# Performance work log

Measured on AMD Instinct MI355X. Metric: run time of the kernel, lower is better.

## Reference

```python
import jax, jax.numpy as jnp
import numpy as np

S = 64.0
M = 0.5
COS_M = float(np.cos(M))
SIN_M = float(np.sin(M))
MM = float(np.sin(M) * M)
THRESHOLD = float(np.cos(np.pi - M))
B, D, V = 2048, 512, 100000


def setup_inputs() -> dict:
    key = jax.random.key(0)
    k1, k2, k3 = jax.random.split(key, 3)
    embeddings = jax.random.normal(k1, (B, D), dtype=jnp.float32)
    labels = jax.random.randint(k2, (B,), 0, V, dtype=jnp.int64)
    # xavier_uniform for [V, D]: limit = sqrt(6/(fan_in+fan_out))
    limit = float(np.sqrt(6.0 / (D + V)))
    weight = jax.random.uniform(k3, (V, D), minval=-limit, maxval=limit, dtype=jnp.float32)
    return {"embeddings": embeddings, "labels": labels, "weight": weight}


def _l2norm(x, axis):
    # matches F.normalize(p=2, eps=1e-12)
    n = jnp.linalg.norm(x, axis=axis, keepdims=True)
    return x / jnp.maximum(n, 1e-12)


def reference(embeddings, labels, weight):
    e = _l2norm(embeddings, axis=1)          # [B, D]
    w = _l2norm(weight, axis=1)              # [V, D]
    cos_theta = jnp.clip(e @ w.T, -1.0, 1.0)  # [B, V]
    sin_theta = jnp.sqrt(jnp.clip(1.0 - cos_theta * cos_theta, 0.0, 1.0))
    cos_theta_m = cos_theta * COS_M - sin_theta * SIN_M
    cos_theta_m = jnp.where(cos_theta > THRESHOLD, cos_theta_m, cos_theta - MM)
    logits = cos_theta_m * S
    logp = jax.nn.log_softmax(logits, axis=1)
    nll = -jnp.take_along_axis(logp, labels[:, None], axis=1)[:, 0]
    return jnp.mean(nll)
```

## Files before the change

kernel.cpp:

```cpp
#include <hip/hip_runtime.h>
#include <hip/hip_bf16.h>
#include <math.h>

#define B_ 2048
#define D_ 512
#define V_ 100000
#define BM 128
#define BN 128
#define NCT 782
#define NBLK (16 * NCT)
#define NBUF 3
#define RED_STRIDE 20

constexpr float S_SCALE = 64.0f;
constexpr float COS_M_ = 0.8775825618903728f;
constexpr float SIN_M_ = 0.479425538604203f;
constexpr float MM_    = 0.2397127693021015f;
constexpr float THRESH = -0.8775825618903728f;
constexpr float LOG2E  = 1.4426950408889634f;
constexpr float LN2    = 0.6931471805599453f;
constexpr float S2     = 64.0f * LOG2E;
constexpr float CMS2   = COS_M_ * S2;
constexpr float SINM_S2= SIN_M_ * S2;
constexpr float KS2    = SINM_S2 * SINM_S2;
constexpr float MMS2   = MM_ * S2;

typedef __attribute__((ext_vector_type(8))) short short8;
typedef __attribute__((ext_vector_type(4))) float f32x4;
typedef __attribute__((ext_vector_type(2))) long long2_t;

__device__ __forceinline__ unsigned short f2bf(float x) {
    __hip_bfloat16 h = __float2bfloat16(x);
    unsigned short u;
    __builtin_memcpy(&u, &h, 2);
    return u;
}

__device__ __forceinline__ void load_lds16(const void* g, void* l) {
    __builtin_amdgcn_global_load_lds(
        (const __attribute__((address_space(1))) unsigned int*)g,
        (__attribute__((address_space(3))) unsigned int*)l,
        16, 0, 0);
}

__device__ __forceinline__ unsigned int pk_fp8x4(float x, float y, float z, float w) {
    int p = __builtin_amdgcn_cvt_pk_fp8_f32(x, y, 0, false);
    p = __builtin_amdgcn_cvt_pk_fp8_f32(z, w, p, true);
    return (unsigned int)p;
}

__device__ __forceinline__ int permj(int j) {
    return (j & ~15) | (((j >> 1) & 3) << 2) | (((j >> 3) & 1) << 1) | (j & 1);
}

__global__ void k_norm_e(const float* __restrict__ e, unsigned short* __restrict__ ebf,
                         unsigned char* __restrict__ ebf8, float* __restrict__ rne,
                         unsigned int* __restrict__ zbuf) {
    if (zbuf && blockIdx.x == 0) zbuf[threadIdx.x] = 0u;
    int row = blockIdx.x * 4 + (threadIdx.x >> 6);
    int lane = threadIdx.x & 63;
    const float4* src = (const float4*)(e + (size_t)row * D_);
    float4 a = src[lane];
    float4 b = src[lane + 64];
    float ss = a.x*a.x + a.y*a.y + a.z*a.z + a.w*a.w
             + b.x*b.x + b.y*b.y + b.z*b.z + b.w*b.w;
    #pragma unroll
    for (int d = 1; d < 64; d <<= 1) ss += __shfl_xor(ss, d, 64);
    float rn = 1.0f / fmaxf(sqrtf(ss), 1e-12f);
    ushort4* dst = (ushort4*)(ebf + (size_t)row * D_);
    dst[lane]      = make_ushort4(f2bf(a.x*rn), f2bf(a.y*rn), f2bf(a.z*rn), f2bf(a.w*rn));
    dst[lane + 64] = make_ushort4(f2bf(b.x*rn), f2bf(b.y*rn), f2bf(b.z*rn), f2bf(b.w*rn));
    if (ebf8) {
        unsigned int* d8 = (unsigned int*)(ebf8 + (size_t)row * D_);
        d8[permj(lane)]      = pk_fp8x4(a.x*rn, a.y*rn, a.z*rn, a.w*rn);
        d8[permj(lane + 64)] = pk_fp8x4(b.x*rn, b.y*rn, b.z*rn, b.w*rn);
    }
    if (lane == 0) rne[row] = rn;
}

__global__ void k_norm_w(const float* __restrict__ w, float* __restrict__ rnw,
                         unsigned char* __restrict__ wbf8) {
    int row = blockIdx.x * 4 + (threadIdx.x >> 6);
    int lane = threadIdx.x & 63;
    const float4* src = (const float4*)(w + (size_t)row * D_);
    float4 a = src[lane];
    float4 b = src[lane + 64];
    float ss = a.x*a.x + a.y*a.y + a.z*a.z + a.w*a.w
             + b.x*b.x + b.y*b.y + b.z*b.z + b.w*b.w;
    #pragma unroll
    for (int d = 1; d < 64; d <<= 1) ss += __shfl_xor(ss, d, 64);
    float rn = 1.0f / fmaxf(sqrtf(ss), 1e-12f);
    if (wbf8) {
        unsigned int* d8 = (unsigned int*)(wbf8 + (size_t)row * D_);
        d8[permj(lane)]      = pk_fp8x4(a.x*rn, a.y*rn, a.z*rn, a.w*rn);
        d8[permj(lane + 64)] = pk_fp8x4(b.x*rn, b.y*rn, b.z*rn, b.w*rn);
    }
    if (lane == 0) rnw[row] = rn;
}

__global__ __launch_bounds__(256, 3) void k_gemm8(const unsigned char* __restrict__ ebf8,
                                                  const unsigned char* __restrict__ wbf8,
                                                  const unsigned char* __restrict__ zbuf,
                                                  float* __restrict__ partials) {
    const int id = blockIdx.x;
    const int wi = (id & 7) * (NBLK / 8) + (id >> 3);
    const int ct = wi >> 4, rt = wi & 15;
    const int row0 = rt * BM, n0 = ct * BN;
    const int tid = threadIdx.x, lane = tid & 63, wid = tid >> 6;
    const int wm = wid >> 1, wn = wid & 1;

    __shared__ __align__(16) unsigned char lds8[NBUF][16384];
    float* red = (float*)&lds8[0][0];

    f32x4 acc[4][4];
    #pragma unroll
    for (int i = 0; i < 4; ++i)
        #pragma unroll
        for (int j = 0; j < 4; ++j)
            acc[i][j] = (f32x4){0.f, 0.f, 0.f, 0.f};

    const int c_ = (lane & 3) ^ ((lane >> 3) & 3);
    const int r0s = wid * 16 + (lane >> 2);
    const unsigned char* gA0 = ebf8 + (size_t)(row0 + r0s) * D_ + c_ * 16;
    const unsigned char* gA1 = ebf8 + (size_t)(row0 + 64 + r0s) * D_ + c_ * 16;
    int gb0 = n0 + r0s, gb1 = n0 + 64 + r0s;
    const unsigned char* gB0 = (gb0 < V_) ? wbf8 + (size_t)gb0 * D_ + c_ * 16 : zbuf + c_ * 16;
    const unsigned char* gB1 = (gb1 < V_) ? wbf8 + (size_t)gb1 * D_ + c_ * 16 : zbuf + c_ * 16;
    const int lb = wid * 1024;

    auto STAGE = [&](int t) {
        unsigned char* Lb = &lds8[t % NBUF][0];
        const int off = t * 64;
        load_lds16(gA0 + off, Lb + lb);
        load_lds16(gA1 + off, Lb + 4096 + lb);
        load_lds16(gB0 + off, Lb + 8192 + lb);
        load_lds16(gB1 + off, Lb + 12288 + lb);
    };

    const int slot = ((lane >> 4) ^ (((lane & 15) >> 1) & 3)) & 3;
    int aoff[4], boff[4];
    #pragma unroll
    for (int mf = 0; mf < 4; ++mf)
        aoff[mf] = (wm * 64 + mf * 16 + (lane & 15)) * 64 + slot * 16;
    #pragma unroll
    for (int nf = 0; nf < 4; ++nf)
        boff[nf] = 8192 + (wn * 64 + nf * 16 + (lane & 15)) * 64 + slot * 16;

    STAGE(0);
    STAGE(1);
    for (int t = 0; t < 8; ++t) {
        if (t < 7) asm volatile("s_waitcnt vmcnt(4)\n\ts_barrier" ::: "memory");
        else       asm volatile("s_waitcnt vmcnt(0)\n\ts_barrier" ::: "memory");
        if (t + 2 < 8) STAGE(t + 2);

        const char* Lb = (const char*)&lds8[t % NBUF][0];
        long2_t a2[4], b2[4];
        #pragma unroll
        for (int mf = 0; mf < 4; ++mf) a2[mf] = *(const long2_t*)(Lb + aoff[mf]);
        #pragma unroll
        for (int nf = 0; nf < 4; ++nf) b2[nf] = *(const long2_t*)(Lb + boff[nf]);
        #pragma unroll
        for (int mf = 0; mf < 4; ++mf)
            #pragma unroll
            for (int nf = 0; nf < 4; ++nf) {
                acc[mf][nf] = __builtin_amdgcn_mfma_f32_16x16x32_fp8_fp8(a2[mf].x, b2[nf].x, acc[mf][nf], 0, 0, 0);
                acc[mf][nf] = __builtin_amdgcn_mfma_f32_16x16x32_fp8_fp8(a2[mf].y, b2[nf].y, acc[mf][nf], 0, 0, 0);
            }
    }
    __syncthreads();

    #pragma unroll
    for (int mf = 0; mf < 4; ++mf) {
        #pragma unroll
        for (int r = 0; r < 4; ++r) {
            float vsum = 0.0f;
            #pragma unroll
            for (int nf = 0; nf < 4; ++nf) {
                float c = acc[mf][nf][r];
                c = __builtin_amdgcn_fmed3f(c, -1.0f, 1.0f);
                float tt = fmaf(-c, c, 1.0f);
                float sts = __builtin_amdgcn_sqrtf(tt * KS2);
                float lgm = fmaf(c, CMS2, -sts);
                float lga = fmaf(c, S2, -MMS2);
                float lg = (c > THRESH) ? lgm : lga;
                vsum += __builtin_amdgcn_exp2f(lg);
            }
            int rowloc = wm * 64 + mf * 16 + (lane >> 4) * 4 + r;
            red[(wn * BM + rowloc) * RED_STRIDE + (lane & 15)] = vsum;
        }
    }
    __syncthreads();
    if (tid < BM) {
        const float4* p0 = (const float4*)(red + (size_t)tid * RED_STRIDE);
        const float4* p1 = (const float4*)(red + (size_t)(BM + tid) * RED_STRIDE);
        float s = 0.0f;
        #pragma unroll
        for (int q = 0; q < 4; ++q) {
            float4 u = p0[q], v = p1[q];
            s += (u.x + u.y) + (u.z + u.w) + (v.x + v.y) + (v.z + v.w);
        }
        partials[(size_t)ct * B_ + row0 + tid] = s;
    }
}

__device__ __forceinline__ int swz64(int row, int col) {
    return (row * 64 + col) ^ ((row & 7) << 3);
}
__global__ __launch_bounds__(256) void k_gemm_fb(const unsigned short* __restrict__ ebf,
                                                 const float* __restrict__ w,
                                                 const float* __restrict__ rnw,
                                                 float* __restrict__ partials) {
    const int rt = blockIdx.x, ct = blockIdx.y;
    const int row0 = rt * BM, n0 = ct * BN;
    const int tid = threadIdx.x, lane = tid & 63, wid = tid >> 6;
    const int wm = wid >> 1, wn = wid & 1;
    __shared__ __align__(16) unsigned short As[BM * 64];
    __shared__ __align__(16) unsigned short Bs[BN * 64];
    float* red = (float*)&As[0];
    f32x4 acc[4][4];
    #pragma unroll
    for (int i = 0; i < 4; ++i)
        #pragma unroll
        for (int j = 0; j < 4; ++j) acc[i][j] = (f32x4){0.f, 0.f, 0.f, 0.f};
    for (int ks = 0; ks < D_ / 64; ++ks) {
        const int kk = ks * 64;
        #pragma unroll
        for (int p = 0; p < 4; ++p) {
            int idx = p * 256 + tid;
            int r = idx >> 3, c = (idx & 7) * 8;
            *(uint4*)(As + swz64(r, c)) = *(const uint4*)(ebf + (size_t)(row0 + r) * D_ + kk + c);
        }
        #pragma unroll
        for (int p = 0; p < 4; ++p) {
            int idx = p * 256 + tid;
            int r = idx >> 3, c = (idx & 7) * 8;
            int gr = n0 + r;
            uint4 val = make_uint4(0, 0, 0, 0);
            if (gr < V_) {
                float rn = rnw[gr];
                const float4* src = (const float4*)(w + (size_t)gr * D_ + kk + c);
                float4 f0 = src[0], f1 = src[1];
                val.x = (unsigned)f2bf(f0.x*rn) | ((unsigned)f2bf(f0.y*rn) << 16);
                val.y = (unsigned)f2bf(f0.z*rn) | ((unsigned)f2bf(f0.w*rn) << 16);
                val.z = (unsigned)f2bf(f1.x*rn) | ((unsigned)f2bf(f1.y*rn) << 16);
                val.w = (unsigned)f2bf(f1.z*rn) | ((unsigned)f2bf(f1.w*rn) << 16);
            }
            *(uint4*)(Bs + swz64(r, c)) = val;
        }
        __syncthreads();
        #pragma unroll
        for (int kc = 0; kc < 2; ++kc) {
            const int kbase = kc * 32 + (lane >> 4) * 8;
            short8 af[4], bfr[4];
            #pragma unroll
            for (int mf = 0; mf < 4; ++mf) af[mf] = *(const short8*)(As + swz64(wm * 64 + mf * 16 + (lane & 15), kbase));
            #pragma unroll
            for (int nf = 0; nf < 4; ++nf) bfr[nf] = *(const short8*)(Bs + swz64(wn * 64 + nf * 16 + (lane & 15), kbase));
            #pragma unroll
            for (int mf = 0; mf < 4; ++mf)
                #pragma unroll
                for (int nf = 0; nf < 4; ++nf)
                    acc[mf][nf] = __builtin_amdgcn_mfma_f32_16x16x32_bf16(af[mf], bfr[nf], acc[mf][nf], 0, 0, 0);
        }
        __syncthreads();
    }
    const int vlim = V_ - n0;
    #pragma unroll
    for (int mf = 0; mf < 4; ++mf) {
        #pragma unroll
        for (int r = 0; r < 4; ++r) {
            float vsum = 0.0f;
            #pragma unroll
            for (int nf = 0; nf < 4; ++nf) {
                float c = acc[mf][nf][r];
                int coltile = wn * 64 + nf * 16 + (lane & 15);
                c = __builtin_amdgcn_fmed3f(c, -1.0f, 1.0f);
                float tt = fmaf(-c, c, 1.0f);
                float sts = __builtin_amdgcn_sqrtf(tt * KS2);
                float lgm = fmaf(c, CMS2, -sts);
                float lga = fmaf(c, S2, -MMS2);
                float lg = (c > THRESH) ? lgm : lga;
                lg = (coltile < vlim) ? lg : -INFINITY;
                vsum += __builtin_amdgcn_exp2f(lg);
            }
            int rowloc = wm * 64 + mf * 16 + (lane >> 4) * 4 + r;
            red[(wn * BM + rowloc) * RED_STRIDE + (lane & 15)] = vsum;
        }
    }
    __syncthreads();
    if (tid < BM) {
        const float4* p0 = (const float4*)(red + (size_t)tid * RED_STRIDE);
        const float4* p1 = (const float4*)(red + (size_t)(BM + tid) * RED_STRIDE);
        float s = 0.0f;
        #pragma unroll
        for (int q = 0; q < 4; ++q) {
            float4 u = p0[q], v = p1[q];
            s += (u.x + u.y) + (u.z + u.w) + (v.x + v.y) + (v.z + v.w);
        }
        partials[(size_t)ct * B_ + row0 + tid] = s;
    }
}

__device__ __forceinline__ int get_label(const int* lab32, int b) {
    bool is64 = true;
    #pragma unroll
    for (int i = 1; i < 16; i += 2) is64 = is64 && (lab32[i] == 0);
    return is64 ? (int)(((const long long*)lab32)[b]) : lab32[b];
}

__global__ void k_row(const float* __restrict__ e, const float* __restrict__ w,
                      const int* __restrict__ labels, const float* __restrict__ rne,
                      const float* __restrict__ rnw, const float* __restrict__ partials,
                      float* __restrict__ row_nll, float padcorr) {
    const int b = blockIdx.x;
    const int tid = threadIdx.x;

    float s = 0.0f;
    for (int ctn = tid; ctn < NCT; ctn += 256) s += partials[(size_t)ctn * B_ + b];
    #pragma unroll
    for (int d = 1; d < 64; d <<= 1) s += __shfl_xor(s, d, 64);
    __shared__ float ss_[4], sd_[4];
    if ((tid & 63) == 0) ss_[tid >> 6] = s;

    int lab = get_label(labels, b);
    const float* ep = e + (size_t)b * D_;
    const float* wp = w + (size_t)lab * D_;
    float dot = ep[tid] * wp[tid] + ep[tid + 256] * wp[tid + 256];
    #pragma unroll
    for (int d = 1; d < 64; d <<= 1) dot += __shfl_xor(dot, d, 64);
    if ((tid & 63) == 0) sd_[tid >> 6] = dot;
    __syncthreads();

    if (tid == 0) {
        float S = (ss_[0] + ss_[1]) + (ss_[2] + ss_[3]) - padcorr;
        float lse = __builtin_amdgcn_logf(S) * LN2;
        float c = (sd_[0] + sd_[1] + sd_[2] + sd_[3]) * rne[b] * rnw[lab];
        c = fminf(fmaxf(c, -1.0f), 1.0f);
        float st = sqrtf(fmaxf(1.0f - c * c, 0.0f));
        float cm = c * COS_M_ - st * SIN_M_;
        cm = (c > THRESH) ? cm : (c - MM_);
        row_nll[b] = lse - cm * S_SCALE;
    }
}

__global__ void k_mean(const float* __restrict__ row_nll, float* __restrict__ out) {
    int tid = threadIdx.x;
    float s = 0.0f;
    for (int i = tid; i < B_; i += 256) s += row_nll[i];
    #pragma unroll
    for (int d = 1; d < 64; d <<= 1) s += __shfl_xor(s, d, 64);
    __shared__ float sb[4];
    if ((tid & 63) == 0) sb[tid >> 6] = s;
    __syncthreads();
    if (tid == 0) out[0] = (sb[0] + sb[1] + sb[2] + sb[3]) / (float)B_;
}

extern "C" void kernel_launch(void* const* d_in, const int* in_sizes, int n_in,
                              void* d_out, int out_size, void* d_ws, size_t ws_size,
                              hipStream_t stream) {
    const float* e      = (const float*)d_in[0];
    const int*   labels = (const int*)d_in[1];
    const float* w      = (const float*)d_in[2];
    float* out = (float*)d_out;
    char* ws = (char*)d_ws;

    unsigned short* ebf = (unsigned short*)ws;
    float* rne          = (float*)(ws + 2097152);
    float* rnw          = (float*)(ws + 2105344);
    float* partials     = (float*)(ws + 2505344);
    float* row_nll      = (float*)(ws + 8911488);
    unsigned int* zbuf  = (unsigned int*)(ws + 8919680);
    unsigned char* ebf8 = (unsigned char*)(ws + 8923776);
    unsigned char* wbf8 = (unsigned char*)(ws + 9972352);
    const size_t NEED_PRE = 9972352 + (size_t)V_ * D_;

    const bool pre = ws_size >= NEED_PRE;
    const float padcorr = pre ? 96.0f * exp2f(-(float)SINM_S2) : 0.0f;

    k_norm_e<<<B_ / 4, 256, 0, stream>>>(e, ebf, pre ? ebf8 : nullptr, rne, pre ? zbuf : nullptr);
    k_norm_w<<<V_ / 4, 256, 0, stream>>>(w, rnw, pre ? wbf8 : nullptr);
    if (pre) {
        k_gemm8<<<NBLK, 256, 0, stream>>>(ebf8, wbf8, (const unsigned char*)zbuf, partials);
    } else {
        dim3 g3(B_ / BM, NCT);
        k_gemm_fb<<<g3, 256, 0, stream>>>(ebf, w, rnw, partials);
    }
    k_row<<<B_, 256, 0, stream>>>(e, w, labels, rne, rnw, partials, row_nll, padcorr);
    k_mean<<<1, 256, 0, stream>>>(row_nll, out);
}
```

Measured before the change: 208.5 us.

## Switch FP8 GEMM to 16x16x128 scaled MFMA with wider K tiles

Replaces the pair of 16x16x32 FP8 MFMAs per K-step with the gfx950 scaled 16x16x128 f8f6f4 MFMA using unit scales. K tiles grow from 64 to 128 bytes, and staging drops from three buffers to two buffers of 32KB each, with a new XOR swizzle. The permuted FP8 layout in the normalize kernels is dropped. Occupancy is lowered to 2 blocks per CU, and the pipeline now waits on all loads each step, so there is less prefetch depth and more LDS per block.

```diff
diff --git a/kernel.cpp b/kernel.cpp
--- a/kernel.cpp
+++ b/kernel.cpp
@@ -9,7 +9,6 @@
 #define BN 128
 #define NCT 782
 #define NBLK (16 * NCT)
-#define NBUF 3
 #define RED_STRIDE 20
 
 constexpr float S_SCALE = 64.0f;
@@ -27,7 +26,7 @@
 
 typedef __attribute__((ext_vector_type(8))) short short8;
 typedef __attribute__((ext_vector_type(4))) float f32x4;
-typedef __attribute__((ext_vector_type(2))) long long2_t;
+typedef __attribute__((ext_vector_type(8))) int i32x8;
 
 __device__ __forceinline__ unsigned short f2bf(float x) {
     __hip_bfloat16 h = __float2bfloat16(x);
@@ -47,10 +46,6 @@
     int p = __builtin_amdgcn_cvt_pk_fp8_f32(x, y, 0, false);
     p = __builtin_amdgcn_cvt_pk_fp8_f32(z, w, p, true);
     return (unsigned int)p;
-}
-
-__device__ __forceinline__ int permj(int j) {
-    return (j & ~15) | (((j >> 1) & 3) << 2) | (((j >> 3) & 1) << 1) | (j & 1);
 }
 
 __global__ void k_norm_e(const float* __restrict__ e, unsigned short* __restrict__ ebf,
@@ -72,8 +67,8 @@
     dst[lane + 64] = make_ushort4(f2bf(b.x*rn), f2bf(b.y*rn), f2bf(b.z*rn), f2bf(b.w*rn));
     if (ebf8) {
         unsigned int* d8 = (unsigned int*)(ebf8 + (size_t)row * D_);
-        d8[permj(lane)]      = pk_fp8x4(a.x*rn, a.y*rn, a.z*rn, a.w*rn);
-        d8[permj(lane + 64)] = pk_fp8x4(b.x*rn, b.y*rn, b.z*rn, b.w*rn);
+        d8[lane]      = pk_fp8x4(a.x*rn, a.y*rn, a.z*rn, a.w*rn);
+        d8[lane + 64] = pk_fp8x4(b.x*rn, b.y*rn, b.z*rn, b.w*rn);
     }
     if (lane == 0) rne[row] = rn;
 }
@@ -92,13 +87,13 @@
     float rn = 1.0f / fmaxf(sqrtf(ss), 1e-12f);
     if (wbf8) {
         unsigned int* d8 = (unsigned int*)(wbf8 + (size_t)row * D_);
-        d8[permj(lane)]      = pk_fp8x4(a.x*rn, a.y*rn, a.z*rn, a.w*rn);
-        d8[permj(lane + 64)] = pk_fp8x4(b.x*rn, b.y*rn, b.z*rn, b.w*rn);
+        d8[lane]      = pk_fp8x4(a.x*rn, a.y*rn, a.z*rn, a.w*rn);
+        d8[lane + 64] = pk_fp8x4(b.x*rn, b.y*rn, b.z*rn, b.w*rn);
     }
     if (lane == 0) rnw[row] = rn;
 }
 
-__global__ __launch_bounds__(256, 3) void k_gemm8(const unsigned char* __restrict__ ebf8,
+__global__ __launch_bounds__(256, 2) void k_gemm8(const unsigned char* __restrict__ ebf8,
                                                   const unsigned char* __restrict__ wbf8,
                                                   const unsigned char* __restrict__ zbuf,
                                                   float* __restrict__ partials) {
@@ -109,7 +104,7 @@
     const int tid = threadIdx.x, lane = tid & 63, wid = tid >> 6;
     const int wm = wid >> 1, wn = wid & 1;
 
-    __shared__ __align__(16) unsigned char lds8[NBUF][16384];
+    __shared__ __align__(16) unsigned char lds8[2][32768];
     float* red = (float*)&lds8[0][0];
 
     f32x4 acc[4][4];
@@ -119,53 +114,67 @@
         for (int j = 0; j < 4; ++j)
             acc[i][j] = (f32x4){0.f, 0.f, 0.f, 0.f};
 
-    const int c_ = (lane & 3) ^ ((lane >> 3) & 3);
-    const int r0s = wid * 16 + (lane >> 2);
-    const unsigned char* gA0 = ebf8 + (size_t)(row0 + r0s) * D_ + c_ * 16;
-    const unsigned char* gA1 = ebf8 + (size_t)(row0 + 64 + r0s) * D_ + c_ * 16;
-    int gb0 = n0 + r0s, gb1 = n0 + 64 + r0s;
-    const unsigned char* gB0 = (gb0 < V_) ? wbf8 + (size_t)gb0 * D_ + c_ * 16 : zbuf + c_ * 16;
-    const unsigned char* gB1 = (gb1 < V_) ? wbf8 + (size_t)gb1 * D_ + c_ * 16 : zbuf + c_ * 16;
-    const int lb = wid * 1024;
+    const int c_ = (lane & 7) ^ ((lane >> 3) & 7);
+    const unsigned char* pA[4];
+    const unsigned char* pB[4];
+    #pragma unroll
+    for (int i = 0; i < 4; ++i) {
+        int r = i * 32 + wid * 8 + (lane >> 3);
+        pA[i] = ebf8 + (size_t)(row0 + r) * D_ + c_ * 16;
+        int gb = n0 + r;
+        pB[i] = (gb < V_) ? wbf8 + (size_t)gb * D_ + c_ * 16 : zbuf + c_ * 16;
+    }
+    const int lbw = wid * 1024;
 
     auto STAGE = [&](int t) {
-        unsigned char* Lb = &lds8[t % NBUF][0];
-        const int off = t * 64;
-        load_lds16(gA0 + off, Lb + lb);
-        load_lds16(gA1 + off, Lb + 4096 + lb);
-        load_lds16(gB0 + off, Lb + 8192 + lb);
-        load_lds16(gB1 + off, Lb + 12288 + lb);
+        unsigned char* Lb = &lds8[t & 1][0];
+        const int off = t * 128;
+        #pragma unroll
+        for (int i = 0; i < 4; ++i) {
+            load_lds16(pA[i] + off, Lb + i * 4096 + lbw);
+            load_lds16(pB[i] + off, Lb + 16384 + i * 4096 + lbw);
+        }
     };
 
-    const int slot = ((lane >> 4) ^ (((lane & 15) >> 1) & 3)) & 3;
+    const int s0 = (((lane >> 4) << 1) ^ (lane & 7)) & 7;
     int aoff[4], boff[4];
     #pragma unroll
     for (int mf = 0; mf < 4; ++mf)
-        aoff[mf] = (wm * 64 + mf * 16 + (lane & 15)) * 64 + slot * 16;
+        aoff[mf] = (wm * 64 + mf * 16 + (lane & 15)) * 128 + s0 * 16;
     #pragma unroll
     for (int nf = 0; nf < 4; ++nf)
-        boff[nf] = 8192 + (wn * 64 + nf * 16 + (lane & 15)) * 64 + slot * 16;
+        boff[nf] = 16384 + (wn * 64 + nf * 16 + (lane & 15)) * 128 + s0 * 16;
 
     STAGE(0);
-    STAGE(1);
-    for (int t = 0; t < 8; ++t) {
-        if (t < 7) asm volatile("s_waitcnt vmcnt(4)\n\ts_barrier" ::: "memory");
-        else       asm volatile("s_waitcnt vmcnt(0)\n\ts_barrier" ::: "memory");
-        if (t + 2 < 8) STAGE(t + 2);
-
-        const char* Lb = (const char*)&lds8[t % NBUF][0];
-        long2_t a2[4], b2[4];
-        #pragma unroll
-        for (int mf = 0; mf < 4; ++mf) a2[mf] = *(const long2_t*)(Lb + aoff[mf]);
-        #pragma unroll
-        for (int nf = 0; nf < 4; ++nf) b2[nf] = *(const long2_t*)(Lb + boff[nf]);
+    for (int t = 0; t < 4; ++t) {
+        asm volatile("s_waitcnt vmcnt(0)\n\ts_barrier" ::: "memory");
+        if (t < 3) STAGE(t + 1);
+
+        const char* Lb = (const char*)&lds8[t & 1][0];
+        i32x8 a8[4], b8[4];
+        #pragma unroll
+        for (int mf = 0; mf < 4; ++mf) {
+            union { i32x8 v; uint4 q[2]; } fa;
+            fa.q[0] = *(const uint4*)(Lb + aoff[mf]);
+            fa.q[1] = *(const uint4*)(Lb + (aoff[mf] ^ 16));
+            a8[mf] = fa.v;
+        }
+        #pragma unroll
+        for (int nf = 0; nf < 4; ++nf) {
+            union { i32x8 v; uint4 q[2]; } fb;
+            fb.q[0] = *(const uint4*)(Lb + boff[nf]);
+            fb.q[1] = *(const uint4*)(Lb + (boff[nf] ^ 16));
+            b8[nf] = fb.v;
+        }
         #pragma unroll
         for (int mf = 0; mf < 4; ++mf)
             #pragma unroll
-            for (int nf = 0; nf < 4; ++nf) {
-                acc[mf][nf] = __builtin_amdgcn_mfma_f32_16x16x32_fp8_fp8(a2[mf].x, b2[nf].x, acc[mf][nf], 0, 0, 0);
-                acc[mf][nf] = __builtin_amdgcn_mfma_f32_16x16x32_fp8_fp8(a2[mf].y, b2[nf].y, acc[mf][nf], 0, 0, 0);
-            }
+            for (int nf = 0; nf < 4; ++nf)
+                acc[mf][nf] = __builtin_amdgcn_mfma_scale_f32_16x16x128_f8f6f4(
+                    a8[mf], b8[nf], acc[mf][nf],
+                    0, 0,
+                    0, 0x7F7F7F7F,
+                    0, 0x7F7F7F7F);
     }
     __syncthreads();
 
```

New measurement: 228.6 us. 9.7% more time.

## Switch FP8 GEMM to 32x32x64 scaled MFMA with new LDS fragment layout

Applied to the files above, without the earlier changes.

Replaces the 16x16x32 FP8 MFMA tiles with the gfx950 32x32x64 f8f6f4 scaled MFMA, using unit scales. The FP8 weight and embedding buffers are now stored in natural order instead of permuted, and the LDS read offsets and swizzle change to load 32-byte fragments. The epilogue and row reduction are adapted to the 32x32 accumulator layout with a wider reduction stride. The goal is fewer MFMA issues and LDS reads per k-step. In exchange, the correctness of the new swizzle and the scale operand must hold, and the reduction buffer uses more LDS.

```diff
diff --git a/kernel.cpp b/kernel.cpp
--- a/kernel.cpp
+++ b/kernel.cpp
@@ -11,6 +11,7 @@
 #define NBLK (16 * NCT)
 #define NBUF 3
 #define RED_STRIDE 20
+#define RSTR2 36
 
 constexpr float S_SCALE = 64.0f;
 constexpr float COS_M_ = 0.8775825618903728f;
@@ -27,7 +28,8 @@
 
 typedef __attribute__((ext_vector_type(8))) short short8;
 typedef __attribute__((ext_vector_type(4))) float f32x4;
-typedef __attribute__((ext_vector_type(2))) long long2_t;
+typedef __attribute__((ext_vector_type(16))) float f32x16;
+typedef __attribute__((ext_vector_type(8))) int i32x8;
 
 __device__ __forceinline__ unsigned short f2bf(float x) {
     __hip_bfloat16 h = __float2bfloat16(x);
@@ -47,10 +49,6 @@
     int p = __builtin_amdgcn_cvt_pk_fp8_f32(x, y, 0, false);
     p = __builtin_amdgcn_cvt_pk_fp8_f32(z, w, p, true);
     return (unsigned int)p;
-}
-
-__device__ __forceinline__ int permj(int j) {
-    return (j & ~15) | (((j >> 1) & 3) << 2) | (((j >> 3) & 1) << 1) | (j & 1);
 }
 
 __global__ void k_norm_e(const float* __restrict__ e, unsigned short* __restrict__ ebf,
@@ -72,8 +70,8 @@
     dst[lane + 64] = make_ushort4(f2bf(b.x*rn), f2bf(b.y*rn), f2bf(b.z*rn), f2bf(b.w*rn));
     if (ebf8) {
         unsigned int* d8 = (unsigned int*)(ebf8 + (size_t)row * D_);
-        d8[permj(lane)]      = pk_fp8x4(a.x*rn, a.y*rn, a.z*rn, a.w*rn);
-        d8[permj(lane + 64)] = pk_fp8x4(b.x*rn, b.y*rn, b.z*rn, b.w*rn);
+        d8[lane]      = pk_fp8x4(a.x*rn, a.y*rn, a.z*rn, a.w*rn);
+        d8[lane + 64] = pk_fp8x4(b.x*rn, b.y*rn, b.z*rn, b.w*rn);
     }
     if (lane == 0) rne[row] = rn;
 }
@@ -92,8 +90,8 @@
     float rn = 1.0f / fmaxf(sqrtf(ss), 1e-12f);
     if (wbf8) {
         unsigned int* d8 = (unsigned int*)(wbf8 + (size_t)row * D_);
-        d8[permj(lane)]      = pk_fp8x4(a.x*rn, a.y*rn, a.z*rn, a.w*rn);
-        d8[permj(lane + 64)] = pk_fp8x4(b.x*rn, b.y*rn, b.z*rn, b.w*rn);
+        d8[lane]      = pk_fp8x4(a.x*rn, a.y*rn, a.z*rn, a.w*rn);
+        d8[lane + 64] = pk_fp8x4(b.x*rn, b.y*rn, b.z*rn, b.w*rn);
     }
     if (lane == 0) rnw[row] = rn;
 }
@@ -112,12 +110,13 @@
     __shared__ __align__(16) unsigned char lds8[NBUF][16384];
     float* red = (float*)&lds8[0][0];
 
-    f32x4 acc[4][4];
-    #pragma unroll
-    for (int i = 0; i < 4; ++i)
-        #pragma unroll
-        for (int j = 0; j < 4; ++j)
-            acc[i][j] = (f32x4){0.f, 0.f, 0.f, 0.f};
+    f32x16 acc[2][2];
+    #pragma unroll
+    for (int i = 0; i < 2; ++i)
+        #pragma unroll
+        for (int j = 0; j < 2; ++j)
+            #pragma unroll
+            for (int q = 0; q < 16; ++q) acc[i][j][q] = 0.0f;
 
     const int c_ = (lane & 3) ^ ((lane >> 3) & 3);
     const int r0s = wid * 16 + (lane >> 2);
@@ -137,14 +136,14 @@
         load_lds16(gB1 + off, Lb + 12288 + lb);
     };
 
-    const int slot = ((lane >> 4) ^ (((lane & 15) >> 1) & 3)) & 3;
-    int aoff[4], boff[4];
-    #pragma unroll
-    for (int mf = 0; mf < 4; ++mf)
-        aoff[mf] = (wm * 64 + mf * 16 + (lane & 15)) * 64 + slot * 16;
-    #pragma unroll
-    for (int nf = 0; nf < 4; ++nf)
-        boff[nf] = 8192 + (wn * 64 + nf * 16 + (lane & 15)) * 64 + slot * 16;
+    const int s1 = ((lane >> 5) << 1) ^ ((lane >> 1) & 3);
+    int aoff[2], boff[2];
+    #pragma unroll
+    for (int mi = 0; mi < 2; ++mi)
+        aoff[mi] = (wm * 64 + mi * 32 + (lane & 31)) * 64 + s1 * 16;
+    #pragma unroll
+    for (int ni = 0; ni < 2; ++ni)
+        boff[ni] = 8192 + (wn * 64 + ni * 32 + (lane & 31)) * 64 + s1 * 16;
 
     STAGE(0);
     STAGE(1);
@@ -154,29 +153,42 @@
         if (t + 2 < 8) STAGE(t + 2);
 
         const char* Lb = (const char*)&lds8[t % NBUF][0];
-        long2_t a2[4], b2[4];
-        #pragma unroll
-        for (int mf = 0; mf < 4; ++mf) a2[mf] = *(const long2_t*)(Lb + aoff[mf]);
-        #pragma unroll
-        for (int nf = 0; nf < 4; ++nf) b2[nf] = *(const long2_t*)(Lb + boff[nf]);
-        #pragma unroll
-        for (int mf = 0; mf < 4; ++mf)
-            #pragma unroll
-            for (int nf = 0; nf < 4; ++nf) {
-                acc[mf][nf] = __builtin_amdgcn_mfma_f32_16x16x32_fp8_fp8(a2[mf].x, b2[nf].x, acc[mf][nf], 0, 0, 0);
-                acc[mf][nf] = __builtin_amdgcn_mfma_f32_16x16x32_fp8_fp8(a2[mf].y, b2[nf].y, acc[mf][nf], 0, 0, 0);
-            }
+        i32x8 a8[2], b8[2];
+        #pragma unroll
+        for (int mi = 0; mi < 2; ++mi) {
+            union { i32x8 v; uint4 q[2]; } fa;
+            fa.q[0] = *(const uint4*)(Lb + aoff[mi]);
+            fa.q[1] = *(const uint4*)(Lb + (aoff[mi] ^ 16));
+            a8[mi] = fa.v;
+        }
+        #pragma unroll
+        for (int ni = 0; ni < 2; ++ni) {
+            union { i32x8 v; uint4 q[2]; } fb;
+            fb.q[0] = *(const uint4*)(Lb + boff[ni]);
+            fb.q[1] = *(const uint4*)(Lb + (boff[ni] ^ 16));
+            b8[ni] = fb.v;
+        }
+        #pragma unroll
+        for (int mi = 0; mi < 2; ++mi)
+            #pragma unroll
+            for (int ni = 0; ni < 2; ++ni)
+                acc[mi][ni] = __builtin_amdgcn_mfma_scale_f32_32x32x64_f8f6f4(
+                    a8[mi], b8[ni], acc[mi][ni],
+                    0, 0,
+                    0, 0x7F7F7F7F,
+                    0, 0x7F7F7F7F);
     }
     __syncthreads();
 
-    #pragma unroll
-    for (int mf = 0; mf < 4; ++mf) {
-        #pragma unroll
-        for (int r = 0; r < 4; ++r) {
+    const int hi4 = (lane >> 5) * 4;
+    #pragma unroll
+    for (int mi = 0; mi < 2; ++mi) {
+        #pragma unroll
+        for (int rg = 0; rg < 16; ++rg) {
             float vsum = 0.0f;
             #pragma unroll
-            for (int nf = 0; nf < 4; ++nf) {
-                float c = acc[mf][nf][r];
+            for (int ni = 0; ni < 2; ++ni) {
+                float c = acc[mi][ni][rg];
                 c = __builtin_amdgcn_fmed3f(c, -1.0f, 1.0f);
                 float tt = fmaf(-c, c, 1.0f);
                 float sts = __builtin_amdgcn_sqrtf(tt * KS2);
@@ -185,19 +197,21 @@
                 float lg = (c > THRESH) ? lgm : lga;
                 vsum += __builtin_amdgcn_exp2f(lg);
             }
-            int rowloc = wm * 64 + mf * 16 + (lane >> 4) * 4 + r;
-            red[(wn * BM + rowloc) * RED_STRIDE + (lane & 15)] = vsum;
+            int rowloc = wm * 64 + mi * 32 + (rg & 3) + 8 * (rg >> 2) + hi4;
+            red[(wn * BM + rowloc) * RSTR2 + (lane & 31)] = vsum;
         }
     }
     __syncthreads();
     if (tid < BM) {
-        const float4* p0 = (const float4*)(red + (size_t)tid * RED_STRIDE);
-        const float4* p1 = (const float4*)(red + (size_t)(BM + tid) * RED_STRIDE);
         float s = 0.0f;
         #pragma unroll
-        for (int q = 0; q < 4; ++q) {
-            float4 u = p0[q], v = p1[q];
-            s += (u.x + u.y) + (u.z + u.w) + (v.x + v.y) + (v.z + v.w);
+        for (int h = 0; h < 2; ++h) {
+            const float4* p = (const float4*)(red + (size_t)(h * BM + tid) * RSTR2);
+            #pragma unroll
+            for (int q = 0; q < 8; ++q) {
+                float4 u = p[q];
+                s += (u.x + u.y) + (u.z + u.w);
+            }
         }
         partials[(size_t)ct * B_ + row0 + tid] = s;
     }
```

After: 200.3 us. 3.9% less time.
